# Optimization experiments

Measured on AMD Instinct MI355X. Metric: run time of the kernel, lower is better.

The kernel has to match this reference:

```python
import math
import jax, jax.numpy as jnp
import numpy as np

B, T, D = 4, 4096, 1024
H = 16            # n_heads
HD = D // H       # head_dim = 64
CAP = int(4096 * 0.125)  # mod capacity k = 512
DFF = int(D * 4 * 2 / 3)  # 2730, per SwiGLU
EPS = 1e-6


def rmsnorm(x, g):
    return x * jax.lax.rsqrt(jnp.mean(x * x, axis=-1, keepdims=True) + EPS) * g


def setup_inputs() -> dict:
    key = jax.random.key(0)
    ks = jax.random.split(key, 9)
    s = lambda k, shape: (jax.random.normal(k, shape, jnp.float32) * 0.02)
    return {
        "x": jax.random.normal(ks[0], (B, T, D), jnp.float32),
        "w_router": s(ks[1], (D,)),          # router Linear(d_model,1,bias=False)
        "W_qkv": s(ks[2], (3 * D, D)),       # torch Linear weight layout [out,in]
        "W_out": s(ks[3], (D, D)),
        "g1": jnp.ones((D,), jnp.float32),   # RMSNorm weights
        "g2": jnp.ones((D,), jnp.float32),
        "W1": s(ks[4], (DFF, D)),
        "W2": s(ks[5], (DFF, D)),
        "W3": s(ks[6], (D, DFF)),
    }


def reference(x, w_router, W_qkv, W_out, g1, g2, W1, W2, W3):
    Bq, Tq, Dq = x.shape
    # --- MoD routing: top-k tokens per sequence (T > capacity) ---
    scores = x @ w_router                         # [B, T]
    _, idx = jax.lax.top_k(scores, CAP)           # [B, k], descending-score order (matches torch.topk)
    x_sel = jnp.take_along_axis(x, idx[:, :, None], axis=1)  # [B, k, D]

    # --- causal attention on the gathered subset ---
    h = rmsnorm(x_sel, g1)
    qkv = (h @ W_qkv.T).reshape(Bq, CAP, 3, H, HD)
    q, k, v = jnp.moveaxis(qkv, 2, 0)             # each [B, k, H, HD]
    att = jnp.einsum('bqhd,bkhd->bhqk', q, k) / math.sqrt(HD)
    mask = jnp.triu(jnp.ones((CAP, CAP), bool), 1)  # causal mask in gathered order
    att = jnp.where(mask, -jnp.inf, att)
    att = jax.nn.softmax(att, axis=-1)
    o = jnp.einsum('bhqk,bkhd->bqhd', att, v).reshape(Bq, CAP, Dq)
    x_attn = o @ W_out.T

    # --- SwiGLU FFN ---
    h2 = rmsnorm(x_sel + x_attn, g2)
    x_ff = (jax.nn.silu(h2 @ W1.T) * (h2 @ W2.T)) @ W3.T

    # --- combine and scatter back into the full sequence ---
    x_proc = x_sel + x_attn + x_ff                # [B, k, D]
    out = x.at[jnp.arange(Bq)[:, None], idx].set(x_proc)
    return out
```

## Files before the change

kernel.cpp:

```cpp
#include <hip/hip_runtime.h>
#include <hip/hip_bf16.h>


#define B_   4
#define T_   4096
#define D_   1024
#define H_   16
#define HD_  64
#define CAP_ 512
#define DFF_ 2730
#define DFFP 2752
#define DFFR 2816
#define M_   (B_*CAP_)

typedef __attribute__((ext_vector_type(8))) short          s16x8;
typedef __attribute__((ext_vector_type(8))) unsigned short u16x8;
typedef __attribute__((ext_vector_type(4))) float          f32x4;

__device__ __forceinline__ float bf2f(unsigned short u) {
    union { float f; unsigned int i; } v; v.i = ((unsigned int)u) << 16; return v.f;
}
__device__ __forceinline__ unsigned short f2bf(float f) {
    union { float f; unsigned int i; } v; v.f = f;
    unsigned int r = v.i + 0x7fffu + ((v.i >> 16) & 1u);
    return (unsigned short)(r >> 16);
}

__device__ __forceinline__ void gload_lds16(const unsigned short* g, unsigned short* l) {
    __builtin_amdgcn_global_load_lds(
        (const __attribute__((address_space(1))) unsigned int*)g,
        (__attribute__((address_space(3))) unsigned int*)l, 16, 0, 0);
}

__global__ __launch_bounds__(256) void k_copyf(const float4* __restrict__ s,
                                               float4* __restrict__ d, int n4) {
    int i = blockIdx.x * 256 + threadIdx.x;
    int st = gridDim.x * 256;
    for (; i < n4; i += st) d[i] = s[i];
}

__global__ __launch_bounds__(256) void k_f2b(const float4* __restrict__ s,
                                             ushort4* __restrict__ d, int n4) {
    int i = blockIdx.x * 256 + threadIdx.x;
    int st = gridDim.x * 256;
    for (; i < n4; i += st) {
        float4 v = s[i];
        ushort4 o;
        o.x = f2bf(v.x); o.y = f2bf(v.y); o.z = f2bf(v.z); o.w = f2bf(v.w);
        d[i] = o;
    }
}

__global__ __launch_bounds__(256) void k_f2b_rowpad(const float* __restrict__ src,
                                                    unsigned short* __restrict__ dst,
                                                    int kc, int rows, int total) {
    int g = blockIdx.x * 256 + threadIdx.x;
    int st = gridDim.x * 256;
    for (; g < total; g += st) {
        int row = g / kc;
        u16x8 v = {0, 0, 0, 0, 0, 0, 0, 0};
        if (row < rows) {
            const float* s = src + ((size_t)g) * 8;
#pragma unroll
            for (int j = 0; j < 2; ++j) {
                float4 f = *(const float4*)(s + 4 * j);
                v[4*j]   = f2bf(f.x); v[4*j+1] = f2bf(f.y);
                v[4*j+2] = f2bf(f.z); v[4*j+3] = f2bf(f.w);
            }
        }
        *(u16x8*)(dst + (size_t)g * 8) = v;
    }
}

__global__ __launch_bounds__(256) void k_f2b_pad(const float* __restrict__ src,
                                                 unsigned short* __restrict__ dst,
                                                 int K, int Kp, int rows) {
    int g = blockIdx.x * 256 + threadIdx.x;
    int ng = rows * (Kp >> 3);
    int st = gridDim.x * 256;
    for (; g < ng; g += st) {
        int row = g / (Kp >> 3);
        int c = (g - row * (Kp >> 3)) << 3;
        const float* s = src + (size_t)row * K + c;
        u16x8 v;
        if (c + 8 <= K) {
#pragma unroll
            for (int j = 0; j < 4; ++j) {
                float2 f = *(const float2*)(s + 2 * j);
                v[2*j] = f2bf(f.x); v[2*j+1] = f2bf(f.y);
            }
        } else {
#pragma unroll
            for (int j = 0; j < 8; ++j) v[j] = (c + j < K) ? f2bf(s[j]) : (unsigned short)0;
        }
        *(u16x8*)(dst + (size_t)row * Kp + c) = v;
    }
}

__global__ __launch_bounds__(256) void k_router(const float* __restrict__ x,
                                                const float* __restrict__ wr,
                                                float* __restrict__ sc) {
    int gw   = (blockIdx.x * 256 + threadIdx.x) >> 6;
    int lane = threadIdx.x & 63;
    const float* row = x + (size_t)gw * D_;
    float s = 0.f;
#pragma unroll
    for (int p = 0; p < 4; ++p) {
        int c = p * 256 + lane * 4;
        float4 xv = *(const float4*)(row + c);
        float4 wv = *(const float4*)(wr + c);
        s += xv.x * wv.x + xv.y * wv.y + xv.z * wv.z + xv.w * wv.w;
    }
#pragma unroll
    for (int o = 32; o; o >>= 1) s += __shfl_xor(s, o);
    if (lane == 0) sc[gw] = s;
}

__global__ __launch_bounds__(1024) void k_topk(const float* __restrict__ sc,
                                               int* __restrict__ idx) {
    __shared__ unsigned int hist[256];
    __shared__ unsigned long long okeys[CAP_];
    __shared__ unsigned int ecand[T_];
    __shared__ unsigned int sprefix;
    __shared__ int skneed;
    __shared__ unsigned int scnt, ecnt;
    int t = threadIdx.x;
    const float* s = sc + (size_t)blockIdx.x * T_;

    unsigned int sb[4], ei[4];
#pragma unroll
    for (int j = 0; j < 4; ++j) {
        int i = j * 1024 + t;
        union { float f; unsigned int u; } v; v.f = s[i];
        unsigned int k = (v.u & 0x80000000u) ? ~v.u : (v.u | 0x80000000u);
        sb[j] = ~k;
        ei[j] = (unsigned int)i;
    }
    if (t == 0) { sprefix = 0; skneed = CAP_; scnt = 0; ecnt = 0; }

#pragma unroll
    for (int rs = 24; rs >= 0; rs -= 8) {
        if (t < 256) hist[t] = 0;
        __syncthreads();
        unsigned int pfx = sprefix;
#pragma unroll
        for (int j = 0; j < 4; ++j) {
            if (((unsigned long long)(sb[j] ^ pfx) >> (rs + 8)) == 0ULL)
                atomicAdd(&hist[(sb[j] >> rs) & 255u], 1u);
        }
        __syncthreads();
        if (t < 64) {
            unsigned int h0 = hist[t * 4], h1 = hist[t * 4 + 1];
            unsigned int h2 = hist[t * 4 + 2], h3 = hist[t * 4 + 3];
            unsigned int lsum = h0 + h1 + h2 + h3;
            unsigned int run = lsum;
#pragma unroll
            for (int d = 1; d < 64; d <<= 1) {
                unsigned int v = __shfl_up(run, d);
                if (t >= d) run += v;
            }
            unsigned int excl = run - lsum;
            int need = skneed;
            if (excl < (unsigned int)need && run >= (unsigned int)need) {
                unsigned int cum = excl;
                int b = t * 4;
                if (cum + h0 < (unsigned int)need) { cum += h0; ++b;
                    if (cum + h1 < (unsigned int)need) { cum += h1; ++b;
                        if (cum + h2 < (unsigned int)need) { cum += h2; ++b; } } }
                sprefix = pfx | ((unsigned int)b << rs);
                skneed = need - (int)cum;
            }
        }
        __syncthreads();
    }

    unsigned int Sstar = sprefix;
    int neq = skneed;
#pragma unroll
    for (int j = 0; j < 4; ++j) {
        if (sb[j] < Sstar) {
            unsigned int p = atomicAdd(&scnt, 1u);
            okeys[p] = ((unsigned long long)sb[j] << 32) | ei[j];
        } else if (sb[j] == Sstar) {
            unsigned int p = atomicAdd(&ecnt, 1u);
            ecand[p] = ei[j];
        }
    }
    __syncthreads();
    if (t == 0) {
        unsigned int base = scnt;
        unsigned int ne = ecnt;
        for (int q = 0; q < neq; ++q) {
            unsigned int mn = 0xffffffffu; int mi = 0;
            for (unsigned int e = 0; e < ne; ++e)
                if (ecand[e] < mn) { mn = ecand[e]; mi = (int)e; }
            okeys[base + q] = ((unsigned long long)Sstar << 32) | mn;
            ecand[mi] = 0xffffffffu;
        }
    }
    __syncthreads();
    if (t < CAP_) {
        unsigned long long mine = okeys[t];
        int r = 0;
#pragma unroll 8
        for (int q = 0; q < CAP_; ++q) r += (okeys[q] < mine) ? 1 : 0;
        idx[blockIdx.x * CAP_ + r] = (int)(mine & 0xffffffffu);
    }
}

__global__ __launch_bounds__(256) void k_gather_rms(const float* __restrict__ x,
                                                    const int* __restrict__ idx,
                                                    const float* __restrict__ g,
                                                    unsigned short* __restrict__ h) {
    int r = blockIdx.x;
    int b = r >> 9;
    int src = idx[r] & (T_ - 1);
    const float* xr = x + ((size_t)b * T_ + src) * D_;
    int c = threadIdx.x * 4;
    float4 xv = *(const float4*)(xr + c);
    float ss = xv.x*xv.x + xv.y*xv.y + xv.z*xv.z + xv.w*xv.w;
#pragma unroll
    for (int o = 32; o; o >>= 1) ss += __shfl_xor(ss, o);
    __shared__ float red[4];
    int lane = threadIdx.x & 63, w = threadIdx.x >> 6;
    if (lane == 0) red[w] = ss;
    __syncthreads();
    float tot = red[0] + red[1] + red[2] + red[3];
    float scale = rsqrtf(tot * (1.f / D_) + 1e-6f);
    float4 gv = *(const float4*)(g + c);
    ushort4 hv;
    hv.x = f2bf(xv.x * scale * gv.x);
    hv.y = f2bf(xv.y * scale * gv.y);
    hv.z = f2bf(xv.z * scale * gv.z);
    hv.w = f2bf(xv.w * scale * gv.w);
    *(ushort4*)(h + (size_t)r * D_ + c) = hv;
}

__global__ __launch_bounds__(256) void k_gemm64g(const unsigned short* __restrict__ A,
                                                 const unsigned short* __restrict__ Bw,
                                                 unsigned short* __restrict__ C,
                                                 int Nout, int Kr) {
    __shared__ __align__(16) unsigned short As[64 * 64];
    __shared__ __align__(16) unsigned short Bs[128 * 64];
    int m0 = blockIdx.x * 64;
    int n0 = blockIdx.y * 128;
    int t = threadIdx.x;
    int w = t >> 6, lane = t & 63;
    int lr = lane & 15, lg = lane >> 4;
    int l8 = lane >> 3, lm8 = lane & 7;

    f32x4 acc[4][2];
#pragma unroll
    for (int mi = 0; mi < 4; ++mi)
#pragma unroll
        for (int ni = 0; ni < 2; ++ni) acc[mi][ni] = {0.f, 0.f, 0.f, 0.f};

    for (int k0 = 0; k0 < Kr; k0 += 64) {
#pragma unroll
        for (int j = 0; j < 2; ++j) {
            int r0 = w * 16 + j * 8;
            int row = r0 + l8;
            int cb = lm8 ^ (row & 7);
            gload_lds16(A + (size_t)(m0 + row) * Kr + k0 + cb * 8, &As[r0 * 64]);
        }
#pragma unroll
        for (int j = 0; j < 4; ++j) {
            int r0 = w * 32 + j * 8;
            int row = r0 + l8;
            int cb = lm8 ^ (row & 7);
            gload_lds16(Bw + (size_t)(n0 + row) * Kr + k0 + cb * 8, &Bs[r0 * 64]);
        }
        __syncthreads();
#pragma unroll
        for (int kh = 0; kh < 2; ++kh) {
            s16x8 af[4], bf[2];
#pragma unroll
            for (int i = 0; i < 4; ++i) {
                int row = i * 16 + lr;
                int pb = (kh * 4 + lg) ^ (row & 7);
                af[i] = *(const s16x8*)&As[row * 64 + pb * 8];
            }
#pragma unroll
            for (int i = 0; i < 2; ++i) {
                int row = w * 32 + i * 16 + lr;
                int pb = (kh * 4 + lg) ^ (row & 7);
                bf[i] = *(const s16x8*)&Bs[row * 64 + pb * 8];
            }
#pragma unroll
            for (int mi = 0; mi < 4; ++mi)
#pragma unroll
                for (int ni = 0; ni < 2; ++ni)
                    acc[mi][ni] = __builtin_amdgcn_mfma_f32_16x16x32_bf16(af[mi], bf[ni],
                                                                          acc[mi][ni], 0, 0, 0);
        }
        __syncthreads();
    }
    int orow0 = m0 + (lg << 2);
    int ocol0 = n0 + w * 32 + lr;
#pragma unroll
    for (int ni = 0; ni < 2; ++ni) {
        int col = ocol0 + ni * 16;
        if (col < Nout) {
#pragma unroll
            for (int mi = 0; mi < 4; ++mi)
#pragma unroll
                for (int i = 0; i < 4; ++i)
                    C[(size_t)(orow0 + mi * 16 + i) * Nout + col] = f2bf(acc[mi][ni][i]);
        }
    }
}

__global__ __launch_bounds__(256) void k_gemm64g2(const unsigned short* __restrict__ A,
                                                  const unsigned short* __restrict__ B1,
                                                  const unsigned short* __restrict__ B2,
                                                  unsigned short* __restrict__ F,
                                                  int Nout, int Kr) {
    __shared__ __align__(16) unsigned short As[64 * 64];
    __shared__ __align__(16) unsigned short B1s[128 * 64];
    __shared__ __align__(16) unsigned short B2s[128 * 64];
    int m0 = blockIdx.x * 64;
    int n0 = blockIdx.y * 128;
    int t = threadIdx.x;
    int w = t >> 6, lane = t & 63;
    int lr = lane & 15, lg = lane >> 4;
    int l8 = lane >> 3, lm8 = lane & 7;

    f32x4 accU[4][2], accG[4][2];
#pragma unroll
    for (int mi = 0; mi < 4; ++mi)
#pragma unroll
        for (int ni = 0; ni < 2; ++ni) {
            accU[mi][ni] = {0.f, 0.f, 0.f, 0.f};
            accG[mi][ni] = {0.f, 0.f, 0.f, 0.f};
        }

    for (int k0 = 0; k0 < Kr; k0 += 64) {
#pragma unroll
        for (int j = 0; j < 2; ++j) {
            int r0 = w * 16 + j * 8;
            int row = r0 + l8;
            int cb = lm8 ^ (row & 7);
            gload_lds16(A + (size_t)(m0 + row) * Kr + k0 + cb * 8, &As[r0 * 64]);
        }
#pragma unroll
        for (int j = 0; j < 4; ++j) {
            int r0 = w * 32 + j * 8;
            int row = r0 + l8;
            int cb = lm8 ^ (row & 7);
            size_t goff = (size_t)(n0 + row) * Kr + k0 + cb * 8;
            gload_lds16(B1 + goff, &B1s[r0 * 64]);
            gload_lds16(B2 + goff, &B2s[r0 * 64]);
        }
        __syncthreads();
#pragma unroll
        for (int kh = 0; kh < 2; ++kh) {
            s16x8 af[4], b1f[2], b2f[2];
#pragma unroll
            for (int i = 0; i < 4; ++i) {
                int row = i * 16 + lr;
                int pb = (kh * 4 + lg) ^ (row & 7);
                af[i] = *(const s16x8*)&As[row * 64 + pb * 8];
            }
#pragma unroll
            for (int i = 0; i < 2; ++i) {
                int row = w * 32 + i * 16 + lr;
                int pb = (kh * 4 + lg) ^ (row & 7);
                b1f[i] = *(const s16x8*)&B1s[row * 64 + pb * 8];
                b2f[i] = *(const s16x8*)&B2s[row * 64 + pb * 8];
            }
#pragma unroll
            for (int mi = 0; mi < 4; ++mi)
#pragma unroll
                for (int ni = 0; ni < 2; ++ni) {
                    accU[mi][ni] = __builtin_amdgcn_mfma_f32_16x16x32_bf16(af[mi], b1f[ni],
                                                                           accU[mi][ni], 0, 0, 0);
                    accG[mi][ni] = __builtin_amdgcn_mfma_f32_16x16x32_bf16(af[mi], b2f[ni],
                                                                           accG[mi][ni], 0, 0, 0);
                }
        }
        __syncthreads();
    }
    int orow0 = m0 + (lg << 2);
    int ocol0 = n0 + w * 32 + lr;
#pragma unroll
    for (int ni = 0; ni < 2; ++ni) {
        int col = ocol0 + ni * 16;
        if (col < Nout) {
#pragma unroll
            for (int mi = 0; mi < 4; ++mi)
#pragma unroll
                for (int i = 0; i < 4; ++i) {
                    float u = accU[mi][ni][i];
                    float sl = u / (1.f + __expf(-u));
                    F[(size_t)(orow0 + mi * 16 + i) * Nout + col] = f2bf(sl * accG[mi][ni][i]);
                }
        }
    }
}

__global__ __launch_bounds__(256) void k_attn_mfma(const unsigned short* __restrict__ qkv,
                                                   unsigned short* __restrict__ o) {
    __shared__ __align__(16) unsigned short Ks[32][72];
    __shared__ __align__(16) unsigned short Vt[64][40];
    __shared__ __align__(16) unsigned short Ps[4][16][40];
    int qt = blockIdx.x, h = blockIdx.y, b = blockIdx.z;
    int q0 = qt * 64;
    int t = threadIdx.x, w = t >> 6, lane = t & 63;
    int lr = lane & 15, lg = lane >> 4;
    const unsigned short* base = qkv + (size_t)b * CAP_ * 3 * D_;

    int qrow = q0 + w * 16 + lr;
    const unsigned short* qp = base + (size_t)qrow * 3 * D_ + h * 64;
    s16x8 aq0 = *(const s16x8*)(qp + lg * 8);
    s16x8 aq1 = *(const s16x8*)(qp + 32 + lg * 8);

    f32x4 zero = {0.f, 0.f, 0.f, 0.f};
    f32x4 oacc[4] = {zero, zero, zero, zero};
    float m_[4], l_[4];
#pragma unroll
    for (int i = 0; i < 4; ++i) { m_[i] = -3.0e38f; l_[i] = 0.f; }

    int qbase = q0 + w * 16 + lg * 4;
    int ntile = (q0 + 64) >> 5;

    int skv = t >> 3, sc = (t & 7) * 8;
    for (int kt = 0; kt < ntile; ++kt) {
        int kv0 = kt << 5;
        {
            const unsigned short* kr = base + (size_t)(kv0 + skv) * 3 * D_ + D_     + h * 64 + sc;
            const unsigned short* vr = base + (size_t)(kv0 + skv) * 3 * D_ + 2 * D_ + h * 64 + sc;
            *(u16x8*)&Ks[skv][sc] = *(const u16x8*)kr;
            u16x8 vv = *(const u16x8*)vr;
#pragma unroll
            for (int j = 0; j < 8; ++j) Vt[sc + j][skv] = vv[j];
        }
        __syncthreads();
        f32x4 s0 = zero, s1 = zero;
        s16x8 k00 = *(const s16x8*)&Ks[lr][lg * 8];
        s16x8 k01 = *(const s16x8*)&Ks[lr][32 + lg * 8];
        s16x8 k10 = *(const s16x8*)&Ks[16 + lr][lg * 8];
        s16x8 k11 = *(const s16x8*)&Ks[16 + lr][32 + lg * 8];
        s0 = __builtin_amdgcn_mfma_f32_16x16x32_bf16(aq0, k00, s0, 0, 0, 0);
        s0 = __builtin_amdgcn_mfma_f32_16x16x32_bf16(aq1, k01, s0, 0, 0, 0);
        s1 = __builtin_amdgcn_mfma_f32_16x16x32_bf16(aq0, k10, s1, 0, 0, 0);
        s1 = __builtin_amdgcn_mfma_f32_16x16x32_bf16(aq1, k11, s1, 0, 0, 0);
#pragma unroll
        for (int i = 0; i < 4; ++i) {
            float v0 = s0[i] * 0.125f, v1 = s1[i] * 0.125f;
            if (kv0 + lr      > qbase + i) v0 = -3.0e38f;
            if (kv0 + 16 + lr > qbase + i) v1 = -3.0e38f;
            s0[i] = v0; s1[i] = v1;
        }
        float pm[4];
#pragma unroll
        for (int i = 0; i < 4; ++i) pm[i] = fmaxf(s0[i], s1[i]);
#pragma unroll
        for (int d = 1; d < 16; d <<= 1) {
#pragma unroll
            for (int i = 0; i < 4; ++i) pm[i] = fmaxf(pm[i], __shfl_xor(pm[i], d));
        }
        float p0[4], p1[4], ps[4], scl[4];
#pragma unroll
        for (int i = 0; i < 4; ++i) {
            float mn = fmaxf(m_[i], pm[i]);
            scl[i] = __expf(m_[i] - mn);
            p0[i] = __expf(s0[i] - mn);
            p1[i] = __expf(s1[i] - mn);
            ps[i] = p0[i] + p1[i];
            m_[i] = mn;
        }
#pragma unroll
        for (int d = 1; d < 16; d <<= 1) {
#pragma unroll
            for (int i = 0; i < 4; ++i) ps[i] += __shfl_xor(ps[i], d);
        }
#pragma unroll
        for (int i = 0; i < 4; ++i) l_[i] = l_[i] * scl[i] + ps[i];
#pragma unroll
        for (int dg = 0; dg < 4; ++dg)
#pragma unroll
            for (int i = 0; i < 4; ++i) oacc[dg][i] *= scl[i];
#pragma unroll
        for (int i = 0; i < 4; ++i) {
            Ps[w][lg * 4 + i][lr]      = f2bf(p0[i]);
            Ps[w][lg * 4 + i][16 + lr] = f2bf(p1[i]);
        }
        __syncthreads();
        s16x8 pa = *(const s16x8*)&Ps[w][lr][lg * 8];
#pragma unroll
        for (int dg = 0; dg < 4; ++dg) {
            s16x8 vf = *(const s16x8*)&Vt[dg * 16 + lr][lg * 8];
            oacc[dg] = __builtin_amdgcn_mfma_f32_16x16x32_bf16(pa, vf, oacc[dg], 0, 0, 0);
        }
        __syncthreads();
    }
    unsigned short* orow = o + ((size_t)(b * CAP_ + qbase)) * D_ + h * 64;
#pragma unroll
    for (int i = 0; i < 4; ++i) {
        float inv = 1.f / l_[i];
#pragma unroll
        for (int dg = 0; dg < 4; ++dg)
            orow[(size_t)i * D_ + dg * 16 + lr] = f2bf(oacc[dg][i] * inv);
    }
}

__global__ __launch_bounds__(256) void k_add_rms(const float* __restrict__ x,
                                                 const int* __restrict__ idx,
                                                 const unsigned short* __restrict__ xattn,
                                                 const float* __restrict__ g,
                                                 unsigned short* __restrict__ y,
                                                 unsigned short* __restrict__ h) {
    int r = blockIdx.x;
    int b = r >> 9;
    int src = idx[r] & (T_ - 1);
    int c = threadIdx.x * 4;
    const float* xr = x + ((size_t)b * T_ + src) * D_;
    float4 xv = *(const float4*)(xr + c);
    size_t off = (size_t)r * D_ + c;
    ushort4 a4 = *(const ushort4*)(xattn + off);
    float v0 = xv.x + bf2f(a4.x);
    float v1 = xv.y + bf2f(a4.y);
    float v2 = xv.z + bf2f(a4.z);
    float v3 = xv.w + bf2f(a4.w);
    float ss = v0*v0 + v1*v1 + v2*v2 + v3*v3;
#pragma unroll
    for (int o = 32; o; o >>= 1) ss += __shfl_xor(ss, o);
    __shared__ float red[4];
    int lane = threadIdx.x & 63, w = threadIdx.x >> 6;
    if (lane == 0) red[w] = ss;
    __syncthreads();
    float tot = red[0] + red[1] + red[2] + red[3];
    float scale = rsqrtf(tot * (1.f / D_) + 1e-6f);
    ushort4 yv;
    yv.x = f2bf(v0); yv.y = f2bf(v1); yv.z = f2bf(v2); yv.w = f2bf(v3);
    *(ushort4*)(y + off) = yv;
    float4 gv = *(const float4*)(g + c);
    ushort4 hv;
    hv.x = f2bf(v0 * scale * gv.x);
    hv.y = f2bf(v1 * scale * gv.y);
    hv.z = f2bf(v2 * scale * gv.z);
    hv.w = f2bf(v3 * scale * gv.w);
    *(ushort4*)(h + off) = hv;
}

__global__ __launch_bounds__(256) void k_scatter(const unsigned short* __restrict__ y,
                                                 const unsigned short* __restrict__ xff,
                                                 const int* __restrict__ idx,
                                                 float* __restrict__ out) {
    int r = blockIdx.x;
    int b = r >> 9;
    int dst = idx[r] & (T_ - 1);
    int c = threadIdx.x * 4;
    size_t src = (size_t)r * D_ + c;
    ushort4 a4 = *(const ushort4*)(y + src);
    ushort4 f4 = *(const ushort4*)(xff + src);
    float4 o4;
    o4.x = bf2f(a4.x) + bf2f(f4.x);
    o4.y = bf2f(a4.y) + bf2f(f4.y);
    o4.z = bf2f(a4.z) + bf2f(f4.z);
    o4.w = bf2f(a4.w) + bf2f(f4.w);
    *(float4*)(out + ((size_t)b * T_ + dst) * D_ + c) = o4;
}

extern "C" void kernel_launch(void* const* d_in, const int* in_sizes, int n_in,
                              void* d_out, int out_size, void* d_ws, size_t ws_size,
                              hipStream_t stream) {
    const float* x     = (const float*)d_in[0];
    const float* w_rt  = (const float*)d_in[1];
    const float* W_qkv = (const float*)d_in[2];
    const float* W_out = (const float*)d_in[3];
    const float* g1    = (const float*)d_in[4];
    const float* g2    = (const float*)d_in[5];
    const float* W1    = (const float*)d_in[6];
    const float* W2    = (const float*)d_in[7];
    const float* W3    = (const float*)d_in[8];
    float* out = (float*)d_out;

    char* p = (char*)d_ws;
    float* scores = (float*)p;
    int*   idx    = (int*)(p + 65536);
    size_t off = 131072;
    const size_t WPAD = (size_t)DFFR * D_;
    unsigned short* WBIG = (unsigned short*)(p + off); off += 2 * WPAD * 2;
    unsigned short* WB2  = WBIG + WPAD;
    unsigned short* R1   = (unsigned short*)(p + off); off += (size_t)M_*3*D_*2;
    unsigned short* R2   = (unsigned short*)(p + off); off += (size_t)M_*D_*2;
    unsigned short* R3   = (unsigned short*)(p + off); off += (size_t)M_*D_*2;
    unsigned short* R4   = (unsigned short*)(p + off); off += (size_t)M_*D_*2;

    unsigned short* h1    = R2;
    unsigned short* qkvb  = R1;
    unsigned short* attno = R2;
    unsigned short* xattn = R3;
    unsigned short* ybuf  = R4;
    unsigned short* h2b   = R2;
    unsigned short* fbuf  = R1;
    unsigned short* xffb  = R3;

    k_copyf<<<2048, 256, 0, stream>>>((const float4*)x, (float4*)out, (B_*T_*D_) / 4);
    k_router<<<(B_*T_) / 4, 256, 0, stream>>>(x, w_rt, scores);
    k_topk<<<B_, 1024, 0, stream>>>(scores, idx);
    k_gather_rms<<<M_, 256, 0, stream>>>(x, idx, g1, h1);
    k_f2b<<<2048, 256, 0, stream>>>((const float4*)W_qkv, (ushort4*)WBIG, (3*D_*D_) / 4);
    k_gemm64g<<<dim3(M_/64, 3*D_/128), 256, 0, stream>>>(h1, WBIG, qkvb, 3*D_, D_);
    k_attn_mfma<<<dim3(CAP_/64, H_, B_), 256, 0, stream>>>(qkvb, attno);
    k_f2b<<<1024, 256, 0, stream>>>((const float4*)W_out, (ushort4*)WBIG, (D_*D_) / 4);
    k_gemm64g<<<dim3(M_/64, D_/128), 256, 0, stream>>>(attno, WBIG, xattn, D_, D_);
    k_add_rms<<<M_, 256, 0, stream>>>(x, idx, xattn, g2, ybuf, h2b);
    k_f2b_rowpad<<<2048, 256, 0, stream>>>(W1, WBIG, D_/8, DFF_, DFFR*(D_/8));
    k_f2b_rowpad<<<2048, 256, 0, stream>>>(W2, WB2,  D_/8, DFF_, DFFR*(D_/8));
    k_gemm64g2<<<dim3(M_/64, DFFR/128), 256, 0, stream>>>(h2b, WBIG, WB2, fbuf,
                                                          DFFP, D_);
    k_f2b_pad<<<2048, 256, 0, stream>>>(W3, WBIG, DFF_, DFFP, D_);
    k_gemm64g<<<dim3(M_/64, D_/128), 256, 0, stream>>>(fbuf, WBIG, xffb, D_, DFFP);
    k_scatter<<<M_, 256, 0, stream>>>(ybuf, xffb, idx, out);
}
```

Measured before the change: 222.6 us.

## Fuse output copy into router kernel and double-buffer GEMM LDS tiles

The router kernel now also copies x into the output, so x is read from memory once instead of twice and one launch goes away. Both GEMM kernels double-buffer their LDS tiles: the next k-tile is prefetched with global_load_lds while MFMAs run on the current one, leaving a single barrier per iteration. The cost is twice the LDS footprint (about 80KB for the dual-weight GEMM), which can lower occupancy.

```diff
diff --git a/kernel.cpp b/kernel.cpp
--- a/kernel.cpp
+++ b/kernel.cpp
@@ -32,11 +32,26 @@
         (__attribute__((address_space(3))) unsigned int*)l, 16, 0, 0);
 }
 
-__global__ __launch_bounds__(256) void k_copyf(const float4* __restrict__ s,
-                                               float4* __restrict__ d, int n4) {
-    int i = blockIdx.x * 256 + threadIdx.x;
-    int st = gridDim.x * 256;
-    for (; i < n4; i += st) d[i] = s[i];
+__global__ __launch_bounds__(256) void k_copy_router(const float* __restrict__ x,
+                                                     const float* __restrict__ wr,
+                                                     float* __restrict__ out,
+                                                     float* __restrict__ sc) {
+    int gw   = (blockIdx.x * 256 + threadIdx.x) >> 6;
+    int lane = threadIdx.x & 63;
+    const float* row = x + (size_t)gw * D_;
+    float* orow = out + (size_t)gw * D_;
+    float s = 0.f;
+#pragma unroll
+    for (int p = 0; p < 4; ++p) {
+        int c = p * 256 + lane * 4;
+        float4 xv = *(const float4*)(row + c);
+        float4 wv = *(const float4*)(wr + c);
+        *(float4*)(orow + c) = xv;
+        s += xv.x * wv.x + xv.y * wv.y + xv.z * wv.z + xv.w * wv.w;
+    }
+#pragma unroll
+    for (int o = 32; o; o >>= 1) s += __shfl_xor(s, o);
+    if (lane == 0) sc[gw] = s;
 }
 
 __global__ __launch_bounds__(256) void k_f2b(const float4* __restrict__ s,
@@ -95,25 +110,6 @@
         }
         *(u16x8*)(dst + (size_t)row * Kp + c) = v;
     }
-}
-
-__global__ __launch_bounds__(256) void k_router(const float* __restrict__ x,
-                                                const float* __restrict__ wr,
-                                                float* __restrict__ sc) {
-    int gw   = (blockIdx.x * 256 + threadIdx.x) >> 6;
-    int lane = threadIdx.x & 63;
-    const float* row = x + (size_t)gw * D_;
-    float s = 0.f;
-#pragma unroll
-    for (int p = 0; p < 4; ++p) {
-        int c = p * 256 + lane * 4;
-        float4 xv = *(const float4*)(row + c);
-        float4 wv = *(const float4*)(wr + c);
-        s += xv.x * wv.x + xv.y * wv.y + xv.z * wv.z + xv.w * wv.w;
-    }
-#pragma unroll
-    for (int o = 32; o; o >>= 1) s += __shfl_xor(s, o);
-    if (lane == 0) sc[gw] = s;
 }
 
 __global__ __launch_bounds__(1024) void k_topk(const float* __restrict__ sc,
@@ -240,8 +236,8 @@
                                                  const unsigned short* __restrict__ Bw,
                                                  unsigned short* __restrict__ C,
                                                  int Nout, int Kr) {
-    __shared__ __align__(16) unsigned short As[64 * 64];
-    __shared__ __align__(16) unsigned short Bs[128 * 64];
+    __shared__ __align__(16) unsigned short As[2][64 * 64];
+    __shared__ __align__(16) unsigned short Bs[2][128 * 64];
     int m0 = blockIdx.x * 64;
     int n0 = blockIdx.y * 128;
     int t = threadIdx.x;
@@ -249,28 +245,37 @@
     int lr = lane & 15, lg = lane >> 4;
     int l8 = lane >> 3, lm8 = lane & 7;
 
+    int arow = w * 16 + l8;
+    int acb0 = lm8 ^ (arow & 7), acb1 = lm8 ^ ((arow + 8) & 7);
+    int brow = w * 32 + l8;
+    int bcb[4];
+#pragma unroll
+    for (int j = 0; j < 4; ++j) bcb[j] = lm8 ^ ((brow + j * 8) & 7);
+
     f32x4 acc[4][2];
 #pragma unroll
     for (int mi = 0; mi < 4; ++mi)
 #pragma unroll
         for (int ni = 0; ni < 2; ++ni) acc[mi][ni] = {0.f, 0.f, 0.f, 0.f};
 
-    for (int k0 = 0; k0 < Kr; k0 += 64) {
-#pragma unroll
-        for (int j = 0; j < 2; ++j) {
-            int r0 = w * 16 + j * 8;
-            int row = r0 + l8;
-            int cb = lm8 ^ (row & 7);
-            gload_lds16(A + (size_t)(m0 + row) * Kr + k0 + cb * 8, &As[r0 * 64]);
-        }
-#pragma unroll
-        for (int j = 0; j < 4; ++j) {
-            int r0 = w * 32 + j * 8;
-            int row = r0 + l8;
-            int cb = lm8 ^ (row & 7);
-            gload_lds16(Bw + (size_t)(n0 + row) * Kr + k0 + cb * 8, &Bs[r0 * 64]);
-        }
-        __syncthreads();
+#define STAGE_G(buf, k0)                                                          \
+    {                                                                             \
+        gload_lds16(A + (size_t)(m0 + arow) * Kr + (k0) + acb0 * 8,               \
+                    &As[buf][(w * 16) * 64]);                                     \
+        gload_lds16(A + (size_t)(m0 + arow + 8) * Kr + (k0) + acb1 * 8,           \
+                    &As[buf][(w * 16 + 8) * 64]);                                 \
+        _Pragma("unroll")                                                         \
+        for (int j = 0; j < 4; ++j)                                               \
+            gload_lds16(Bw + (size_t)(n0 + brow + j * 8) * Kr + (k0) + bcb[j] * 8,\
+                        &Bs[buf][(w * 32 + j * 8) * 64]);                         \
+    }
+
+    int nk = Kr >> 6;
+    STAGE_G(0, 0);
+    __syncthreads();
+    for (int kt = 0; kt < nk; ++kt) {
+        int cur = kt & 1;
+        if (kt + 1 < nk) STAGE_G(cur ^ 1, (kt + 1) << 6);
 #pragma unroll
         for (int kh = 0; kh < 2; ++kh) {
             s16x8 af[4], bf[2];
@@ -278,13 +283,13 @@
             for (int i = 0; i < 4; ++i) {
                 int row = i * 16 + lr;
                 int pb = (kh * 4 + lg) ^ (row & 7);
-                af[i] = *(const s16x8*)&As[row * 64 + pb * 8];
+                af[i] = *(const s16x8*)&As[cur][row * 64 + pb * 8];
             }
 #pragma unroll
             for (int i = 0; i < 2; ++i) {
                 int row = w * 32 + i * 16 + lr;
                 int pb = (kh * 4 + lg) ^ (row & 7);
-                bf[i] = *(const s16x8*)&Bs[row * 64 + pb * 8];
+                bf[i] = *(const s16x8*)&Bs[cur][row * 64 + pb * 8];
             }
 #pragma unroll
             for (int mi = 0; mi < 4; ++mi)
@@ -295,6 +300,7 @@
         }
         __syncthreads();
     }
+#undef STAGE_G
     int orow0 = m0 + (lg << 2);
     int ocol0 = n0 + w * 32 + lr;
 #pragma unroll
@@ -315,9 +321,9 @@
                                                   const unsigned short* __restrict__ B2,
                                                   unsigned short* __restrict__ F,
                                                   int Nout, int Kr) {
-    __shared__ __align__(16) unsigned short As[64 * 64];
-    __shared__ __align__(16) unsigned short B1s[128 * 64];
-    __shared__ __align__(16) unsigned short B2s[128 * 64];
+    __shared__ __align__(16) unsigned short As[2][64 * 64];
+    __shared__ __align__(16) unsigned short B1s[2][128 * 64];
+    __shared__ __align__(16) unsigned short B2s[2][128 * 64];
     int m0 = blockIdx.x * 64;
     int n0 = blockIdx.y * 128;
     int t = threadIdx.x;
@@ -325,6 +331,13 @@
     int lr = lane & 15, lg = lane >> 4;
     int l8 = lane >> 3, lm8 = lane & 7;
 
+    int arow = w * 16 + l8;
+    int acb0 = lm8 ^ (arow & 7), acb1 = lm8 ^ ((arow + 8) & 7);
+    int brow = w * 32 + l8;
+    int bcb[4];
+#pragma unroll
+    for (int j = 0; j < 4; ++j) bcb[j] = lm8 ^ ((brow + j * 8) & 7);
+
     f32x4 accU[4][2], accG[4][2];
 #pragma unroll
     for (int mi = 0; mi < 4; ++mi)
@@ -334,24 +347,26 @@
             accG[mi][ni] = {0.f, 0.f, 0.f, 0.f};
         }
 
-    for (int k0 = 0; k0 < Kr; k0 += 64) {
-#pragma unroll
-        for (int j = 0; j < 2; ++j) {
-            int r0 = w * 16 + j * 8;
-            int row = r0 + l8;
-            int cb = lm8 ^ (row & 7);
-            gload_lds16(A + (size_t)(m0 + row) * Kr + k0 + cb * 8, &As[r0 * 64]);
-        }
-#pragma unroll
-        for (int j = 0; j < 4; ++j) {
-            int r0 = w * 32 + j * 8;
-            int row = r0 + l8;
-            int cb = lm8 ^ (row & 7);
-            size_t goff = (size_t)(n0 + row) * Kr + k0 + cb * 8;
-            gload_lds16(B1 + goff, &B1s[r0 * 64]);
-            gload_lds16(B2 + goff, &B2s[r0 * 64]);
-        }
-        __syncthreads();
+#define STAGE_G2(buf, k0)                                                          \
+    {                                                                              \
+        gload_lds16(A + (size_t)(m0 + arow) * Kr + (k0) + acb0 * 8,                \
+                    &As[buf][(w * 16) * 64]);                                      \
+        gload_lds16(A + (size_t)(m0 + arow + 8) * Kr + (k0) + acb1 * 8,            \
+                    &As[buf][(w * 16 + 8) * 64]);                                  \
+        _Pragma("unroll")                                                          \
+        for (int j = 0; j < 4; ++j) {                                              \
+            size_t goff = (size_t)(n0 + brow + j * 8) * Kr + (k0) + bcb[j] * 8;    \
+            gload_lds16(B1 + goff, &B1s[buf][(w * 32 + j * 8) * 64]);              \
+            gload_lds16(B2 + goff, &B2s[buf][(w * 32 + j * 8) * 64]);              \
+        }                                                                          \
+    }
+
+    int nk = Kr >> 6;
+    STAGE_G2(0, 0);
+    __syncthreads();
+    for (int kt = 0; kt < nk; ++kt) {
+        int cur = kt & 1;
+        if (kt + 1 < nk) STAGE_G2(cur ^ 1, (kt + 1) << 6);
 #pragma unroll
         for (int kh = 0; kh < 2; ++kh) {
             s16x8 af[4], b1f[2], b2f[2];
@@ -359,14 +374,14 @@
             for (int i = 0; i < 4; ++i) {
                 int row = i * 16 + lr;
                 int pb = (kh * 4 + lg) ^ (row & 7);
-                af[i] = *(const s16x8*)&As[row * 64 + pb * 8];
+                af[i] = *(const s16x8*)&As[cur][row * 64 + pb * 8];
             }
 #pragma unroll
             for (int i = 0; i < 2; ++i) {
                 int row = w * 32 + i * 16 + lr;
                 int pb = (kh * 4 + lg) ^ (row & 7);
-                b1f[i] = *(const s16x8*)&B1s[row * 64 + pb * 8];
-                b2f[i] = *(const s16x8*)&B2s[row * 64 + pb * 8];
+                b1f[i] = *(const s16x8*)&B1s[cur][row * 64 + pb * 8];
+                b2f[i] = *(const s16x8*)&B2s[cur][row * 64 + pb * 8];
             }
 #pragma unroll
             for (int mi = 0; mi < 4; ++mi)
@@ -380,6 +395,7 @@
         }
         __syncthreads();
     }
+#undef STAGE_G2
     int orow0 = m0 + (lg << 2);
     int ocol0 = n0 + w * 32 + lr;
 #pragma unroll
@@ -597,8 +613,7 @@
     unsigned short* fbuf  = R1;
     unsigned short* xffb  = R3;
 
-    k_copyf<<<2048, 256, 0, stream>>>((const float4*)x, (float4*)out, (B_*T_*D_) / 4);
-    k_router<<<(B_*T_) / 4, 256, 0, stream>>>(x, w_rt, scores);
+    k_copy_router<<<(B_*T_) / 4, 256, 0, stream>>>(x, w_rt, out, scores);
     k_topk<<<B_, 1024, 0, stream>>>(scores, idx);
     k_gather_rms<<<M_, 256, 0, stream>>>(x, idx, g1, h1);
     k_f2b<<<2048, 256, 0, stream>>>((const float4*)W_qkv, (ushort4*)WBIG, (3*D_*D_) / 4);
```

New measurement: 216.3 us. 2.8% less time.
